# Optimization experiments

Hardware: AMD Instinct MI355X
Metric: run time of the kernel (lower is better)

## Reference

```python
import jax, jax.numpy as jnp
import numpy as np

EPS = 1e-12  # torch.nn.functional.normalize default eps


def setup_inputs() -> dict:
    key = jax.random.key(0)
    k1, k2 = jax.random.split(key)
    S, P, N, D = 16, 8, 64, 128
    input_data1 = jax.random.normal(k1, (S, P, N, D), dtype=jnp.float32)
    input_data2 = jax.random.normal(k2, (S, P, N, D), dtype=jnp.float32)
    return {"input_data1": input_data1, "input_data2": input_data2}


def _compare(x, y):
    # x, y: [S, P, N, D]; replaces the double python loop over (S, P)
    S, P, N, D = x.shape
    # cos: row-normalize then gram matrix per (s, p) block -> [S, P, N, N]
    xn = x / jnp.maximum(jnp.linalg.norm(x, axis=-1, keepdims=True), EPS)
    yn = y / jnp.maximum(jnp.linalg.norm(y, axis=-1, keepdims=True), EPS)
    cos = jnp.einsum('spnd,spmd->spnm', xn, yn)
    # pairwise differences: [S, P, N, N, D]
    diff = x[:, :, :, None, :] - y[:, :, None, :, :]
    l2 = jnp.sqrt(jnp.sum(diff * diff, axis=-1))   # torch.cdist(p=2)
    l1 = jnp.sum(jnp.abs(diff), axis=-1)           # torch.cdist(p=1)
    # per-block: cat([cos, l2, l1], dim=1) on [N*N, 1] columns -> [N*N, 3]
    out = jnp.stack([cos, l2, l1], axis=-1)        # [S, P, N, N, 3]
    return out.reshape(S, P * N * N, 3)            # result.reshape(S, -1, 3)


def reference(input_data1, input_data2):
    return _compare(input_data1, input_data2)
```

## Files before the change

### kernel.cpp

```cpp
#include <hip/hip_runtime.h>
#include <hip/hip_bf16.h>

namespace {

constexpr int kN = 64;
constexpr int kF4 = 32;
constexpr int kStride = kF4 + 1;
constexpr int kXRows = 32;

__global__ __launch_bounds__(256, 2)
void vcmp_kernel(const float* __restrict__ x, const float* __restrict__ y,
                 float* __restrict__ out) {
  __shared__ float4 xs[kXRows * kStride];
  __shared__ float4 ys[kN * kStride];
  __shared__ float xn2[kXRows], xrn[kXRows];
  __shared__ float yn2[kN], yrn[kN];

  const int tid = threadIdx.x;
  const int bid = blockIdx.x;
  const int sp  = bid >> 1;
  const int r0  = (bid & 1) << 5;

  const float4* gx = reinterpret_cast<const float4*>(x) + ((size_t)sp * kN + r0) * kF4;
  const float4* gy = reinterpret_cast<const float4*>(y) + (size_t)sp * kN * kF4;

  #pragma unroll
  for (int i = tid; i < kXRows * kF4; i += 256) {
    xs[(i >> 5) * kStride + (i & 31)] = gx[i];
  }
  #pragma unroll
  for (int i = tid; i < kN * kF4; i += 256) {
    ys[(i >> 5) * kStride + (i & 31)] = gy[i];
  }
  __syncthreads();

  if (tid < kXRows + kN) {
    const float4* row = (tid < kXRows) ? (xs + tid * kStride)
                                       : (ys + (tid - kXRows) * kStride);
    float s = 0.f;
    #pragma unroll
    for (int c = 0; c < kF4; ++c) {
      const float4 v = row[c];
      s = fmaf(v.x, v.x, s); s = fmaf(v.y, v.y, s);
      s = fmaf(v.z, v.z, s); s = fmaf(v.w, v.w, s);
    }
    const float rn = 1.f / fmaxf(sqrtf(s), 1e-12f);
    if (tid < kXRows) { xn2[tid] = s; xrn[tid] = rn; }
    else              { yn2[tid - kXRows] = s; yrn[tid - kXRows] = rn; }
  }
  __syncthreads();

  const int tn = tid >> 4;
  const int tm = tid & 15;
  const int n0 = tn << 1;

  float dot0[4] = {0.f, 0.f, 0.f, 0.f};
  float dot1[4] = {0.f, 0.f, 0.f, 0.f};
  float l10 [4] = {0.f, 0.f, 0.f, 0.f};
  float l11 [4] = {0.f, 0.f, 0.f, 0.f};
  const float4* xrow0 = xs + n0 * kStride;
  const float4* xrow1 = xrow0 + kStride;

  #pragma unroll 2
  for (int c = 0; c < kF4; ++c) {
    const float4 a0 = xrow0[c];
    const float4 a1 = xrow1[c];
    #pragma unroll
    for (int j = 0; j < 4; ++j) {
      const float4 b = ys[(tm + 16 * j) * kStride + c];
      dot0[j] = fmaf(a0.x, b.x, dot0[j]);
      dot0[j] = fmaf(a0.y, b.y, dot0[j]);
      dot0[j] = fmaf(a0.z, b.z, dot0[j]);
      dot0[j] = fmaf(a0.w, b.w, dot0[j]);
      dot1[j] = fmaf(a1.x, b.x, dot1[j]);
      dot1[j] = fmaf(a1.y, b.y, dot1[j]);
      dot1[j] = fmaf(a1.z, b.z, dot1[j]);
      dot1[j] = fmaf(a1.w, b.w, dot1[j]);
      l10[j] += fabsf(a0.x - b.x);
      l10[j] += fabsf(a0.y - b.y);
      l10[j] += fabsf(a0.z - b.z);
      l10[j] += fabsf(a0.w - b.w);
      l11[j] += fabsf(a1.x - b.x);
      l11[j] += fabsf(a1.y - b.y);
      l11[j] += fabsf(a1.z - b.z);
      l11[j] += fabsf(a1.w - b.w);
    }
  }

  #pragma unroll
  for (int r = 0; r < 2; ++r) {
    const int nl = n0 + r;
    const float nx2 = xn2[nl];
    const float rnx = xrn[nl];
    const float* dt = r ? dot1 : dot0;
    const float* lo = r ? l11  : l10;
    float* op = out + (size_t)(sp * kN + r0 + nl) * kN * 3;
    #pragma unroll
    for (int j = 0; j < 4; ++j) {
      const int m = tm + 16 * j;
      const float d2 = fmaxf(nx2 + yn2[m] - 2.f * dt[j], 0.f);
      float3 v;
      v.x = dt[j] * rnx * yrn[m];
      v.y = sqrtf(d2);
      v.z = lo[j];
      *reinterpret_cast<float3*>(op + (size_t)m * 3) = v;
    }
  }
}

}

extern "C" void kernel_launch(void* const* d_in, const int* in_sizes, int n_in,
                              void* d_out, int out_size, void* d_ws, size_t ws_size,
                              hipStream_t stream) {
  const float* x = (const float*)d_in[0];
  const float* y = (const float*)d_in[1];
  float* out = (float*)d_out;
  vcmp_kernel<<<dim3(256), dim3(256), 0, stream>>>(x, y, out);
}
```

Before: 70.19 us.

## Split each block into 32x32 tiles, doubling grid, and parallelize row norms

Each (s,p) pair is now covered by four blocks, each handling a 32x32 tile of x rows against y rows instead of a 32x64 tile. This doubles the grid to 512 blocks for better occupancy across CUs and halves the shared memory per block. The cost is that each x and y row is loaded twice from global memory. Row norms are computed by four threads per row with shuffle reductions instead of one thread per row, and the inner loop is unrolled further with fewer accumulators per thread.

```diff
diff --git a/kernel.cpp b/kernel.cpp
--- a/kernel.cpp
+++ b/kernel.cpp
@@ -1,52 +1,58 @@
 #include <hip/hip_runtime.h>
-#include <hip/hip_bf16.h>
 
 namespace {
 
 constexpr int kN = 64;
 constexpr int kF4 = 32;
 constexpr int kStride = kF4 + 1;
-constexpr int kXRows = 32;
+constexpr int kRows = 32;
 
 __global__ __launch_bounds__(256, 2)
 void vcmp_kernel(const float* __restrict__ x, const float* __restrict__ y,
                  float* __restrict__ out) {
-  __shared__ float4 xs[kXRows * kStride];
-  __shared__ float4 ys[kN * kStride];
-  __shared__ float xn2[kXRows], xrn[kXRows];
-  __shared__ float yn2[kN], yrn[kN];
+  __shared__ float4 xs[kRows * kStride];
+  __shared__ float4 ys[kRows * kStride];
+  __shared__ float xn2[kRows], xrn[kRows];
+  __shared__ float yn2[kRows], yrn[kRows];
 
   const int tid = threadIdx.x;
   const int bid = blockIdx.x;
-  const int sp  = bid >> 1;
-  const int r0  = (bid & 1) << 5;
+  const int sp  = bid >> 2;
+  const int xr0 = ((bid >> 1) & 1) << 5;
+  const int yr0 = (bid & 1) << 5;
 
-  const float4* gx = reinterpret_cast<const float4*>(x) + ((size_t)sp * kN + r0) * kF4;
-  const float4* gy = reinterpret_cast<const float4*>(y) + (size_t)sp * kN * kF4;
+  const float4* gx = reinterpret_cast<const float4*>(x) + ((size_t)sp * kN + xr0) * kF4;
+  const float4* gy = reinterpret_cast<const float4*>(y) + ((size_t)sp * kN + yr0) * kF4;
 
   #pragma unroll
-  for (int i = tid; i < kXRows * kF4; i += 256) {
+  for (int i = tid; i < kRows * kF4; i += 256) {
     xs[(i >> 5) * kStride + (i & 31)] = gx[i];
   }
   #pragma unroll
-  for (int i = tid; i < kN * kF4; i += 256) {
+  for (int i = tid; i < kRows * kF4; i += 256) {
     ys[(i >> 5) * kStride + (i & 31)] = gy[i];
   }
   __syncthreads();
 
-  if (tid < kXRows + kN) {
-    const float4* row = (tid < kXRows) ? (xs + tid * kStride)
-                                       : (ys + (tid - kXRows) * kStride);
+  {
+    const int row  = tid >> 2;
+    const int part = tid & 3;
+    const float4* src = (row < kRows) ? (xs + row * kStride)
+                                      : (ys + (row - kRows) * kStride);
     float s = 0.f;
     #pragma unroll
-    for (int c = 0; c < kF4; ++c) {
-      const float4 v = row[c];
+    for (int c = 0; c < 8; ++c) {
+      const float4 v = src[part * 8 + c];
       s = fmaf(v.x, v.x, s); s = fmaf(v.y, v.y, s);
       s = fmaf(v.z, v.z, s); s = fmaf(v.w, v.w, s);
     }
-    const float rn = 1.f / fmaxf(sqrtf(s), 1e-12f);
-    if (tid < kXRows) { xn2[tid] = s; xrn[tid] = rn; }
-    else              { yn2[tid - kXRows] = s; yrn[tid - kXRows] = rn; }
+    s += __shfl_xor(s, 1);
+    s += __shfl_xor(s, 2);
+    if (part == 0) {
+      const float rn = 1.f / fmaxf(sqrtf(s), 1e-12f);
+      if (row < kRows) { xn2[row] = s;         xrn[row] = rn; }
+      else             { yn2[row - kRows] = s; yrn[row - kRows] = rn; }
+    }
   }
   __syncthreads();
 
@@ -54,58 +60,68 @@
   const int tm = tid & 15;
   const int n0 = tn << 1;
 
-  float dot0[4] = {0.f, 0.f, 0.f, 0.f};
-  float dot1[4] = {0.f, 0.f, 0.f, 0.f};
-  float l10 [4] = {0.f, 0.f, 0.f, 0.f};
-  float l11 [4] = {0.f, 0.f, 0.f, 0.f};
-  const float4* xrow0 = xs + n0 * kStride;
-  const float4* xrow1 = xrow0 + kStride;
+  const float4* __restrict__ xa0 = xs + n0 * kStride;
+  const float4* __restrict__ xa1 = xa0 + kStride;
+  const float4* __restrict__ yb0 = ys + tm * kStride;
+  const float4* __restrict__ yb1 = ys + (tm + 16) * kStride;
 
-  #pragma unroll 2
+  float dot00 = 0.f, dot01 = 0.f, dot10 = 0.f, dot11 = 0.f;
+  float l1_00 = 0.f, l1_01 = 0.f, l1_10 = 0.f, l1_11 = 0.f;
+
+  #pragma unroll 8
   for (int c = 0; c < kF4; ++c) {
-    const float4 a0 = xrow0[c];
-    const float4 a1 = xrow1[c];
-    #pragma unroll
-    for (int j = 0; j < 4; ++j) {
-      const float4 b = ys[(tm + 16 * j) * kStride + c];
-      dot0[j] = fmaf(a0.x, b.x, dot0[j]);
-      dot0[j] = fmaf(a0.y, b.y, dot0[j]);
-      dot0[j] = fmaf(a0.z, b.z, dot0[j]);
-      dot0[j] = fmaf(a0.w, b.w, dot0[j]);
-      dot1[j] = fmaf(a1.x, b.x, dot1[j]);
-      dot1[j] = fmaf(a1.y, b.y, dot1[j]);
-      dot1[j] = fmaf(a1.z, b.z, dot1[j]);
-      dot1[j] = fmaf(a1.w, b.w, dot1[j]);
-      l10[j] += fabsf(a0.x - b.x);
-      l10[j] += fabsf(a0.y - b.y);
-      l10[j] += fabsf(a0.z - b.z);
-      l10[j] += fabsf(a0.w - b.w);
-      l11[j] += fabsf(a1.x - b.x);
-      l11[j] += fabsf(a1.y - b.y);
-      l11[j] += fabsf(a1.z - b.z);
-      l11[j] += fabsf(a1.w - b.w);
-    }
+    const float4 a0 = xa0[c];
+    const float4 a1 = xa1[c];
+    const float4 b0 = yb0[c];
+    const float4 b1 = yb1[c];
+
+    dot00 = fmaf(a0.x, b0.x, dot00); dot00 = fmaf(a0.y, b0.y, dot00);
+    dot00 = fmaf(a0.z, b0.z, dot00); dot00 = fmaf(a0.w, b0.w, dot00);
+    dot01 = fmaf(a0.x, b1.x, dot01); dot01 = fmaf(a0.y, b1.y, dot01);
+    dot01 = fmaf(a0.z, b1.z, dot01); dot01 = fmaf(a0.w, b1.w, dot01);
+    dot10 = fmaf(a1.x, b0.x, dot10); dot10 = fmaf(a1.y, b0.y, dot10);
+    dot10 = fmaf(a1.z, b0.z, dot10); dot10 = fmaf(a1.w, b0.w, dot10);
+    dot11 = fmaf(a1.x, b1.x, dot11); dot11 = fmaf(a1.y, b1.y, dot11);
+    dot11 = fmaf(a1.z, b1.z, dot11); dot11 = fmaf(a1.w, b1.w, dot11);
+
+    l1_00 += fabsf(a0.x - b0.x); l1_00 += fabsf(a0.y - b0.y);
+    l1_00 += fabsf(a0.z - b0.z); l1_00 += fabsf(a0.w - b0.w);
+    l1_01 += fabsf(a0.x - b1.x); l1_01 += fabsf(a0.y - b1.y);
+    l1_01 += fabsf(a0.z - b1.z); l1_01 += fabsf(a0.w - b1.w);
+    l1_10 += fabsf(a1.x - b0.x); l1_10 += fabsf(a1.y - b0.y);
+    l1_10 += fabsf(a1.z - b0.z); l1_10 += fabsf(a1.w - b0.w);
+    l1_11 += fabsf(a1.x - b1.x); l1_11 += fabsf(a1.y - b1.y);
+    l1_11 += fabsf(a1.z - b1.z); l1_11 += fabsf(a1.w - b1.w);
   }
 
-  #pragma unroll
-  for (int r = 0; r < 2; ++r) {
-    const int nl = n0 + r;
-    const float nx2 = xn2[nl];
-    const float rnx = xrn[nl];
-    const float* dt = r ? dot1 : dot0;
-    const float* lo = r ? l11  : l10;
-    float* op = out + (size_t)(sp * kN + r0 + nl) * kN * 3;
-    #pragma unroll
-    for (int j = 0; j < 4; ++j) {
-      const int m = tm + 16 * j;
-      const float d2 = fmaxf(nx2 + yn2[m] - 2.f * dt[j], 0.f);
-      float3 v;
-      v.x = dt[j] * rnx * yrn[m];
-      v.y = sqrtf(d2);
-      v.z = lo[j];
-      *reinterpret_cast<float3*>(op + (size_t)m * 3) = v;
-    }
-  }
+  const float nx2_0 = xn2[n0],     rnx_0 = xrn[n0];
+  const float nx2_1 = xn2[n0 + 1], rnx_1 = xrn[n0 + 1];
+  const float ny2_0 = yn2[tm],      rny_0 = yrn[tm];
+  const float ny2_1 = yn2[tm + 16], rny_1 = yrn[tm + 16];
+
+  float* orow0 = out + ((size_t)(sp * kN + xr0 + n0) * kN + yr0) * 3;
+  float* orow1 = orow0 + (size_t)kN * 3;
+
+  float3 v;
+  v.x = dot00 * rnx_0 * rny_0;
+  v.y = sqrtf(fmaxf(nx2_0 + ny2_0 - 2.f * dot00, 0.f));
+  v.z = l1_00;
+  *reinterpret_cast<float3*>(orow0 + (size_t)tm * 3) = v;
+
+  v.x = dot01 * rnx_0 * rny_1;
+  v.y = sqrtf(fmaxf(nx2_0 + ny2_1 - 2.f * dot01, 0.f));
+  v.z = l1_01;
+  *reinterpret_cast<float3*>(orow0 + (size_t)(tm + 16) * 3) = v;
+
+  v.x = dot10 * rnx_1 * rny_0;
+  v.y = sqrtf(fmaxf(nx2_1 + ny2_0 - 2.f * dot10, 0.f));
+  v.z = l1_10;
+  *reinterpret_cast<float3*>(orow1 + (size_t)tm * 3) = v;
+
+  v.x = dot11 * rnx_1 * rny_1;
+  v.y = sqrtf(fmaxf(nx2_1 + ny2_1 - 2.f * dot11, 0.f));
+  v.z = l1_11;
+  *reinterpret_cast<float3*>(orow1 + (size_t)(tm + 16) * 3) = v;
 }
 
 }
@@ -116,5 +132,5 @@
   const float* x = (const float*)d_in[0];
   const float* y = (const float*)d_in[1];
   float* out = (float*)d_out;
-  vcmp_kernel<<<dim3(256), dim3(256), 0, stream>>>(x, y, out);
+  vcmp_kernel<<<dim3(512), dim3(256), 0, stream>>>(x, y, out);
 }
```

New measurement: 69.61 us. About the same (-0.8%).
